# Kernel tuning notes

Hardware: AMD Instinct MI355X
Metric: run time of the kernel (lower is better)

The kernel has to match this reference:

```python
import jax, jax.numpy as jnp
import numpy as np

HINGES = 8_000_000
SHIMS = 2
L = 1.0


def setup_inputs() -> dict:
    key = jax.random.key(0)
    k1, k2, k3 = jax.random.split(key, 3)
    # straight chain [[0,0],[1,0],...] + small perturbation (as in _initiate_pos)
    x = jnp.arange(HINGES + 2, dtype=jnp.float32)
    base = jnp.stack([x, jnp.zeros_like(x)], axis=1)
    pos_arr = base + 0.01 * jax.random.normal(k1, (HINGES + 2, 2), dtype=jnp.float32)
    thetas_ss = 0.3 * jax.random.uniform(k2, (HINGES,), dtype=jnp.float32)
    rest_lengths = jnp.full((HINGES + 1,), L, dtype=jnp.float32)
    # buckle in {-1, +1}
    buckle = (2 * jax.random.randint(k3, (HINGES, SHIMS), 0, 2) - 1).astype(jnp.int32)
    return {
        "pos_arr": pos_arr,
        "thetas_ss": thetas_ss,
        "rest_lengths": rest_lengths,
        "k_stiff": jnp.asarray(10.0, dtype=jnp.float32),
        "k_soft": jnp.asarray(0.1, dtype=jnp.float32),
        "k_stretch": jnp.asarray(100.0, dtype=jnp.float32),
        "buckle": buckle,
    }


def _energy(pos, thetas_ss, rest_lengths, k_stiff, k_soft, k_stretch, buckle):
    # hinge angles: signed angle between consecutive edge vectors (vmap'd _get_theta)
    v1 = pos[1:-1] - pos[:-2]   # (H, 2)
    v2 = pos[2:] - pos[1:-1]    # (H, 2)
    cross = v1[:, 0] * v2[:, 1] - v1[:, 1] * v2[:, 0]
    dot = jnp.sum(v1 * v2, axis=-1)
    thetas = jnp.arctan2(cross, dot)             # (H,)
    # edge lengths (vmap'd _get_edge_length), edges = hinges + 1
    ev = pos[1:] - pos[:-1]
    edge_len = jnp.sqrt(jnp.sum(ev * ev, axis=-1))  # (H+1,)

    T = thetas[:, None]          # (H, 1)
    TH = thetas_ss[:, None]      # (H, 1)
    B = buckle                   # (H, shims)
    stiff_mask = ((B == 1) & (T > -TH)) | ((B == -1) & (T < TH))
    k_rot = jnp.where(stiff_mask, k_stiff, k_soft)
    rot_e = 0.5 * jnp.sum(k_rot * (T - TH) ** 2)
    str_e = 0.5 * jnp.sum(k_stretch * (edge_len - rest_lengths) ** 2)
    return rot_e + str_e, rot_e, str_e


def reference(pos_arr, thetas_ss, rest_lengths, k_stiff, k_soft, k_stretch, buckle):
    n_coords = pos_arr.size
    # nodes 0 and 1 (DOFs 0..3) are constrained per calculate_state
    free = jnp.ones((n_coords,), dtype=bool).at[:4].set(False)

    def total_E(x_flat):
        p = x_flat.reshape(pos_arr.shape)
        return _energy(p, thetas_ss, rest_lengths, k_stiff, k_soft, k_stretch, buckle)[0]

    g = jax.grad(total_E)(pos_arr.reshape(-1))
    force = jnp.where(free, -g, 0.0)             # -dE/dx on free DOFs

    tot, rot, st = _energy(pos_arr, thetas_ss, rest_lengths, k_stiff, k_soft, k_stretch, buckle)
    energies = jnp.stack([tot, rot, st])
    return jnp.concatenate([energies, force])
```

## Files before the change

kernel.cpp:

```cpp
#include <hip/hip_runtime.h>
#include <math.h>

#define TILE 256
#define PPT  4

__device__ __forceinline__ float fast_rcp(float x) { return __builtin_amdgcn_rcpf(x); }
__device__ __forceinline__ float fast_rsq(float x) { return __builtin_amdgcn_rsqf(x); }

__device__ __forceinline__ float atan_poly(float t) {
    const float c3 = -0.3333333333f, c5 = 0.2f, c7 = -0.1428571429f, c9 = 0.1111111111f;
    float t2 = t * t;
    return t * fmaf(t2, fmaf(t2, fmaf(t2, fmaf(t2, c9, c7), c5), c3), 1.0f);
}

__global__ __launch_bounds__(TILE) void hinge_chain_kernel(
    const float2* __restrict__ pos,
    const float*  __restrict__ thetas_ss,
    const float*  __restrict__ rest_len,
    const float*  __restrict__ k_stiff_p,
    const float*  __restrict__ k_soft_p,
    const float*  __restrict__ k_stretch_p,
    const int2*   __restrict__ buckle,
    float*        __restrict__ out,
    float2*       __restrict__ partials,
    int N)
{
    const int H = N - 2;
    const int E = N - 1;
    const int gid = blockIdx.x * TILE + threadIdx.x;
    const int p0  = gid * PPT;

    const float k_stiff   = *k_stiff_p;
    const float k_soft    = *k_soft_p;
    const float k_stretch = *k_stretch_p;

    float2 P[8];
    float  tss[6];
    int2   bb[6];
    float  rl[5];

    const bool interior = (p0 >= 2) && (p0 + 5 < N);
    if (interior) {
        const float4* p4 = reinterpret_cast<const float4*>(pos + (p0 - 2));
        float4 a = p4[0], b = p4[1], c = p4[2], d = p4[3];
        P[0] = make_float2(a.x, a.y); P[1] = make_float2(a.z, a.w);
        P[2] = make_float2(b.x, b.y); P[3] = make_float2(b.z, b.w);
        P[4] = make_float2(c.x, c.y); P[5] = make_float2(c.z, c.w);
        P[6] = make_float2(d.x, d.y); P[7] = make_float2(d.z, d.w);
        float2 t01 = *reinterpret_cast<const float2*>(thetas_ss + (p0 - 2));
        float4 t25 = *reinterpret_cast<const float4*>(thetas_ss + p0);
        tss[0] = t01.x; tss[1] = t01.y;
        tss[2] = t25.x; tss[3] = t25.y; tss[4] = t25.z; tss[5] = t25.w;
        rl[0] = rest_len[p0 - 1];
        float4 r14 = *reinterpret_cast<const float4*>(rest_len + p0);
        rl[1] = r14.x; rl[2] = r14.y; rl[3] = r14.z; rl[4] = r14.w;
        const int4* b4 = reinterpret_cast<const int4*>(buckle + (p0 - 2));
        int4 u = b4[0], v = b4[1], w = b4[2];
        bb[0] = make_int2(u.x, u.y); bb[1] = make_int2(u.z, u.w);
        bb[2] = make_int2(v.x, v.y); bb[3] = make_int2(v.z, v.w);
        bb[4] = make_int2(w.x, w.y); bb[5] = make_int2(w.z, w.w);
    } else {
        #pragma unroll
        for (int j = 0; j < 8; ++j) {
            int p = p0 - 2 + j;
            P[j] = (p >= 0 && p < N) ? pos[p] : make_float2(0.f, 0.f);
        }
        #pragma unroll
        for (int j = 0; j < 6; ++j) {
            int h = p0 - 2 + j;
            bool v = (h >= 0 && h < H);
            tss[j] = v ? thetas_ss[h] : 0.f;
            bb[j]  = v ? buckle[h]    : make_int2(0, 0);
        }
        #pragma unroll
        for (int k = 0; k < 5; ++k) {
            int e = p0 - 1 + k;
            rl[k] = (e >= 0 && e < E) ? rest_len[e] : 1.f;
        }
    }

    float rot_e = 0.f, str_e = 0.f;

    float2 g1[6], g2[6];
    #pragma unroll
    for (int j = 0; j < 6; ++j) {
        int h = p0 - 2 + j;
        bool valid = (h >= 0 && h < H);
        if (valid) {
            float2 a = P[j], b = P[j + 1], c = P[j + 2];
            float v1x = b.x - a.x, v1y = b.y - a.y;
            float v2x = c.x - b.x, v2y = c.y - b.y;
            float cr = v1x * v2y - v1y * v2x;
            float dt = v1x * v2x + v1y * v2y;
            float th;
            if (dt > 0.f) th = atan_poly(cr * fast_rcp(dt));
            else          th = atan2f(cr, dt);
            float ts  = tss[j];
            int2  bk  = bb[j];
            float dth = th - ts;
            bool m0 = (bk.x == 1 && th > -ts) || (bk.x == -1 && th < ts);
            bool m1 = (bk.y == 1 && th > -ts) || (bk.y == -1 && th < ts);
            float K = (m0 ? k_stiff : k_soft) + (m1 ? k_stiff : k_soft);
            if (j >= 2) rot_e += 0.5f * K * dth * dth;
            float gg  = K * dth;
            float inv = gg * fast_rcp(cr * cr + dt * dt);
            g1[j].x = inv * ( dt * v2y - cr * v2x);
            g1[j].y = inv * (-dt * v2x - cr * v2y);
            g2[j].x = inv * (-dt * v1y - cr * v1x);
            g2[j].y = inv * ( dt * v1x - cr * v1y);
        } else {
            g1[j] = make_float2(0.f, 0.f);
            g2[j] = make_float2(0.f, 0.f);
        }
    }

    float2 s[5];
    #pragma unroll
    for (int k = 0; k < 5; ++k) {
        int e = p0 - 1 + k;
        bool valid = (e >= 0 && e < E);
        if (valid) {
            float2 a = P[k + 1], b = P[k + 2];
            float ex = b.x - a.x, ey = b.y - a.y;
            float d2 = ex * ex + ey * ey;
            float invl = fast_rsq(d2);
            float len  = d2 * invl;
            float d    = len - rl[k];
            if (k >= 1) str_e += 0.5f * k_stretch * d * d;
            float cc = k_stretch * d * invl;
            s[k] = make_float2(cc * ex, cc * ey);
        } else {
            s[k] = make_float2(0.f, 0.f);
        }
    }

    #pragma unroll
    for (int m = 0; m < 4; ++m) {
        int p = p0 + m;
        if (p < N) {
            float gx = -g1[m + 2].x + g1[m + 1].x - g2[m + 1].x + g2[m].x + s[m].x - s[m + 1].x;
            float gy = -g1[m + 2].y + g1[m + 1].y - g2[m + 1].y + g2[m].y + s[m].y - s[m + 1].y;
            float fx = -gx, fy = -gy;
            if (p < 2) { fx = 0.f; fy = 0.f; }
            out[3 + 2 * p]     = fx;
            out[4 + 2 * p]     = fy;
        }
    }

    for (int off = 32; off > 0; off >>= 1) {
        rot_e += __shfl_down(rot_e, off);
        str_e += __shfl_down(str_e, off);
    }
    __shared__ float wr[TILE / 64], wsum[TILE / 64];
    int wave = threadIdx.x >> 6, lane = threadIdx.x & 63;
    if (lane == 0) { wr[wave] = rot_e; wsum[wave] = str_e; }
    __syncthreads();
    if (threadIdx.x == 0) {
        float r = 0.f, ss = 0.f;
        for (int w = 0; w < TILE / 64; ++w) { r += wr[w]; ss += wsum[w]; }
        partials[blockIdx.x] = make_float2(r, ss);
    }
}

__global__ __launch_bounds__(256) void reduce_partials_kernel(
    const float2* __restrict__ partials, int nblocks,
    float* __restrict__ out)
{
    const int tid = threadIdx.x;
    float r0 = 0.f, s0 = 0.f, r1 = 0.f, s1 = 0.f;
    int i = tid;
    for (; i + 256 < nblocks; i += 512) {
        float2 a = partials[i];
        float2 b = partials[i + 256];
        r0 += a.x; s0 += a.y;
        r1 += b.x; s1 += b.y;
    }
    if (i < nblocks) { float2 a = partials[i]; r0 += a.x; s0 += a.y; }
    float r = r0 + r1, s = s0 + s1;
    for (int off = 32; off > 0; off >>= 1) {
        r += __shfl_down(r, off);
        s += __shfl_down(s, off);
    }
    __shared__ float wr[4], wsv[4];
    int wave = tid >> 6, lane = tid & 63;
    if (lane == 0) { wr[wave] = r; wsv[wave] = s; }
    __syncthreads();
    if (tid == 0) {
        float R = 0.f, S = 0.f;
        for (int w = 0; w < 4; ++w) { R += wr[w]; S += wsv[w]; }
        out[0] = R + S;
        out[1] = R;
        out[2] = S;
    }
}

extern "C" void kernel_launch(void* const* d_in, const int* in_sizes, int n_in,
                              void* d_out, int out_size, void* d_ws, size_t ws_size,
                              hipStream_t stream) {
    const float2* pos       = (const float2*)d_in[0];
    const float*  thetas_ss = (const float*)d_in[1];
    const float*  rest_len  = (const float*)d_in[2];
    const float*  k_stiff   = (const float*)d_in[3];
    const float*  k_soft    = (const float*)d_in[4];
    const float*  k_stretch = (const float*)d_in[5];
    const int2*   buckle    = (const int2*)d_in[6];
    float*        out       = (float*)d_out;
    float2*       partials  = (float2*)d_ws;

    const int N = in_sizes[0] / 2;
    const int nthreads = (N + PPT - 1) / PPT;
    const int grid = (nthreads + TILE - 1) / TILE;

    hinge_chain_kernel<<<grid, TILE, 0, stream>>>(
        pos, thetas_ss, rest_len, k_stiff, k_soft, k_stretch, buckle, out, partials, N);

    reduce_partials_kernel<<<1, 256, 0, stream>>>(partials, grid, out);
}
```

Before: 223.8 us.

## Switch to persistent grid-stride loop with double-buffered chunk prefetch

Replaces the one-chunk-per-thread launch with a fixed grid of 1024 blocks that walk chunks in a grid-stride loop. Each thread loads the next chunk into a second register buffer while it computes the current one, so memory latency overlaps with math. The change also cuts the partials array and the final reduce work to 1024 entries. In exchange it roughly doubles register use per thread, which is capped through launch bounds and may cause spills or lower occupancy.

Measured after the change: 234.5 us. +4.8%, slower.

```diff
diff --git a/kernel.cpp b/kernel.cpp
--- a/kernel.cpp
+++ b/kernel.cpp
@@ -3,6 +3,7 @@
 
 #define TILE 256
 #define PPT  4
+#define NBLK 1024
 
 __device__ __forceinline__ float fast_rcp(float x) { return __builtin_amdgcn_rcpf(x); }
 __device__ __forceinline__ float fast_rsq(float x) { return __builtin_amdgcn_rsqf(x); }
@@ -13,73 +14,68 @@
     return t * fmaf(t2, fmaf(t2, fmaf(t2, fmaf(t2, c9, c7), c5), c3), 1.0f);
 }
 
-__global__ __launch_bounds__(TILE) void hinge_chain_kernel(
-    const float2* __restrict__ pos,
-    const float*  __restrict__ thetas_ss,
-    const float*  __restrict__ rest_len,
-    const float*  __restrict__ k_stiff_p,
-    const float*  __restrict__ k_soft_p,
-    const float*  __restrict__ k_stretch_p,
-    const int2*   __restrict__ buckle,
-    float*        __restrict__ out,
-    float2*       __restrict__ partials,
-    int N)
-{
-    const int H = N - 2;
-    const int E = N - 1;
-    const int gid = blockIdx.x * TILE + threadIdx.x;
-    const int p0  = gid * PPT;
-
-    const float k_stiff   = *k_stiff_p;
-    const float k_soft    = *k_soft_p;
-    const float k_stretch = *k_stretch_p;
-
+struct Chunk {
     float2 P[8];
     float  tss[6];
     int2   bb[6];
     float  rl[5];
-
+};
+
+__device__ __forceinline__ void loadChunk(
+    Chunk& ch, int c, int N, int H, int E,
+    const float2* __restrict__ pos,
+    const float*  __restrict__ thetas_ss,
+    const float*  __restrict__ rest_len,
+    const int2*   __restrict__ buckle)
+{
+    const int p0 = c * PPT;
     const bool interior = (p0 >= 2) && (p0 + 5 < N);
     if (interior) {
         const float4* p4 = reinterpret_cast<const float4*>(pos + (p0 - 2));
-        float4 a = p4[0], b = p4[1], c = p4[2], d = p4[3];
-        P[0] = make_float2(a.x, a.y); P[1] = make_float2(a.z, a.w);
-        P[2] = make_float2(b.x, b.y); P[3] = make_float2(b.z, b.w);
-        P[4] = make_float2(c.x, c.y); P[5] = make_float2(c.z, c.w);
-        P[6] = make_float2(d.x, d.y); P[7] = make_float2(d.z, d.w);
+        float4 a = p4[0], b = p4[1], cc = p4[2], d = p4[3];
+        ch.P[0] = make_float2(a.x, a.y);  ch.P[1] = make_float2(a.z, a.w);
+        ch.P[2] = make_float2(b.x, b.y);  ch.P[3] = make_float2(b.z, b.w);
+        ch.P[4] = make_float2(cc.x, cc.y); ch.P[5] = make_float2(cc.z, cc.w);
+        ch.P[6] = make_float2(d.x, d.y);  ch.P[7] = make_float2(d.z, d.w);
         float2 t01 = *reinterpret_cast<const float2*>(thetas_ss + (p0 - 2));
         float4 t25 = *reinterpret_cast<const float4*>(thetas_ss + p0);
-        tss[0] = t01.x; tss[1] = t01.y;
-        tss[2] = t25.x; tss[3] = t25.y; tss[4] = t25.z; tss[5] = t25.w;
-        rl[0] = rest_len[p0 - 1];
+        ch.tss[0] = t01.x; ch.tss[1] = t01.y;
+        ch.tss[2] = t25.x; ch.tss[3] = t25.y; ch.tss[4] = t25.z; ch.tss[5] = t25.w;
+        ch.rl[0] = rest_len[p0 - 1];
         float4 r14 = *reinterpret_cast<const float4*>(rest_len + p0);
-        rl[1] = r14.x; rl[2] = r14.y; rl[3] = r14.z; rl[4] = r14.w;
+        ch.rl[1] = r14.x; ch.rl[2] = r14.y; ch.rl[3] = r14.z; ch.rl[4] = r14.w;
         const int4* b4 = reinterpret_cast<const int4*>(buckle + (p0 - 2));
         int4 u = b4[0], v = b4[1], w = b4[2];
-        bb[0] = make_int2(u.x, u.y); bb[1] = make_int2(u.z, u.w);
-        bb[2] = make_int2(v.x, v.y); bb[3] = make_int2(v.z, v.w);
-        bb[4] = make_int2(w.x, w.y); bb[5] = make_int2(w.z, w.w);
+        ch.bb[0] = make_int2(u.x, u.y); ch.bb[1] = make_int2(u.z, u.w);
+        ch.bb[2] = make_int2(v.x, v.y); ch.bb[3] = make_int2(v.z, v.w);
+        ch.bb[4] = make_int2(w.x, w.y); ch.bb[5] = make_int2(w.z, w.w);
     } else {
         #pragma unroll
         for (int j = 0; j < 8; ++j) {
             int p = p0 - 2 + j;
-            P[j] = (p >= 0 && p < N) ? pos[p] : make_float2(0.f, 0.f);
+            ch.P[j] = (p >= 0 && p < N) ? pos[p] : make_float2(0.f, 0.f);
         }
         #pragma unroll
         for (int j = 0; j < 6; ++j) {
             int h = p0 - 2 + j;
             bool v = (h >= 0 && h < H);
-            tss[j] = v ? thetas_ss[h] : 0.f;
-            bb[j]  = v ? buckle[h]    : make_int2(0, 0);
+            ch.tss[j] = v ? thetas_ss[h] : 0.f;
+            ch.bb[j]  = v ? buckle[h]    : make_int2(0, 0);
         }
         #pragma unroll
         for (int k = 0; k < 5; ++k) {
             int e = p0 - 1 + k;
-            rl[k] = (e >= 0 && e < E) ? rest_len[e] : 1.f;
-        }
-    }
-
-    float rot_e = 0.f, str_e = 0.f;
+            ch.rl[k] = (e >= 0 && e < E) ? rest_len[e] : 1.f;
+        }
+    }
+}
+
+__device__ __forceinline__ void computeStore(
+    const Chunk& ch, int c, int N, int H, int E,
+    float k_stiff, float k_soft, float k_stretch,
+    float* __restrict__ out, float& rot_e, float& str_e)
+{
+    const int p0 = c * PPT;
 
     float2 g1[6], g2[6];
     #pragma unroll
@@ -87,16 +83,16 @@
         int h = p0 - 2 + j;
         bool valid = (h >= 0 && h < H);
         if (valid) {
-            float2 a = P[j], b = P[j + 1], c = P[j + 2];
-            float v1x = b.x - a.x, v1y = b.y - a.y;
-            float v2x = c.x - b.x, v2y = c.y - b.y;
+            float2 a = ch.P[j], b = ch.P[j + 1], cpt = ch.P[j + 2];
+            float v1x = b.x - a.x,   v1y = b.y - a.y;
+            float v2x = cpt.x - b.x, v2y = cpt.y - b.y;
             float cr = v1x * v2y - v1y * v2x;
             float dt = v1x * v2x + v1y * v2y;
             float th;
             if (dt > 0.f) th = atan_poly(cr * fast_rcp(dt));
             else          th = atan2f(cr, dt);
-            float ts  = tss[j];
-            int2  bk  = bb[j];
+            float ts  = ch.tss[j];
+            int2  bk  = ch.bb[j];
             float dth = th - ts;
             bool m0 = (bk.x == 1 && th > -ts) || (bk.x == -1 && th < ts);
             bool m1 = (bk.y == 1 && th > -ts) || (bk.y == -1 && th < ts);
@@ -120,12 +116,12 @@
         int e = p0 - 1 + k;
         bool valid = (e >= 0 && e < E);
         if (valid) {
-            float2 a = P[k + 1], b = P[k + 2];
+            float2 a = ch.P[k + 1], b = ch.P[k + 2];
             float ex = b.x - a.x, ey = b.y - a.y;
             float d2 = ex * ex + ey * ey;
             float invl = fast_rsq(d2);
             float len  = d2 * invl;
-            float d    = len - rl[k];
+            float d    = len - ch.rl[k];
             if (k >= 1) str_e += 0.5f * k_stretch * d * d;
             float cc = k_stretch * d * invl;
             s[k] = make_float2(cc * ex, cc * ey);
@@ -142,9 +138,53 @@
             float gy = -g1[m + 2].y + g1[m + 1].y - g2[m + 1].y + g2[m].y + s[m].y - s[m + 1].y;
             float fx = -gx, fy = -gy;
             if (p < 2) { fx = 0.f; fy = 0.f; }
-            out[3 + 2 * p]     = fx;
-            out[4 + 2 * p]     = fy;
-        }
+            out[3 + 2 * p] = fx;
+            out[4 + 2 * p] = fy;
+        }
+    }
+}
+
+__global__ __launch_bounds__(TILE, 4) void hinge_chain_kernel(
+    const float2* __restrict__ pos,
+    const float*  __restrict__ thetas_ss,
+    const float*  __restrict__ rest_len,
+    const float*  __restrict__ k_stiff_p,
+    const float*  __restrict__ k_soft_p,
+    const float*  __restrict__ k_stretch_p,
+    const int2*   __restrict__ buckle,
+    float*        __restrict__ out,
+    float2*       __restrict__ partials,
+    int N)
+{
+    const int H = N - 2;
+    const int E = N - 1;
+    const int C = (N + PPT - 1) / PPT;
+    const int T = gridDim.x * TILE;
+
+    const float k_stiff   = *k_stiff_p;
+    const float k_soft    = *k_soft_p;
+    const float k_stretch = *k_stretch_p;
+
+    float rot_e = 0.f, str_e = 0.f;
+
+    Chunk A, B;
+    int  c     = blockIdx.x * TILE + threadIdx.x;
+    bool valid = (c < C);
+    if (valid) loadChunk(A, c, N, H, E, pos, thetas_ss, rest_len, buckle);
+
+    while (valid) {
+        int  cn = c + T;
+        bool vn = (cn < C);
+        if (vn) loadChunk(B, cn, N, H, E, pos, thetas_ss, rest_len, buckle);
+        computeStore(A, c, N, H, E, k_stiff, k_soft, k_stretch, out, rot_e, str_e);
+        c = cn; valid = vn;
+        if (!valid) break;
+
+        cn = c + T;
+        vn = (cn < C);
+        if (vn) loadChunk(A, cn, N, H, E, pos, thetas_ss, rest_len, buckle);
+        computeStore(B, c, N, H, E, k_stiff, k_soft, k_stretch, out, rot_e, str_e);
+        c = cn; valid = vn;
     }
 
     for (int off = 32; off > 0; off >>= 1) {
@@ -208,8 +248,9 @@
     float2*       partials  = (float2*)d_ws;
 
     const int N = in_sizes[0] / 2;
-    const int nthreads = (N + PPT - 1) / PPT;
-    const int grid = (nthreads + TILE - 1) / TILE;
+    const int nchunks = (N + PPT - 1) / PPT;
+    int grid = NBLK;
+    if (grid * TILE > nchunks) grid = (nchunks + TILE - 1) / TILE;
 
     hinge_chain_kernel<<<grid, TILE, 0, stream>>>(
         pos, thetas_ss, rest_len, k_stiff, k_soft, k_stretch, buckle, out, partials, N);
```

## Stage block inputs into LDS via async global_load_lds before compute

Applied to the files above, without the earlier changes.

Each block now copies its whole span of positions, thetas, rest lengths and buckle values into shared memory using 16-byte global_load_lds transfers, with a guarded scalar fallback at the edges, then reads per-thread windows from LDS. This replaces overlapping per-thread global loads, where neighbouring threads re-fetch halo elements, with one coalesced bulk copy per block. In exchange it adds about 28 KB of LDS per block, which can lower occupancy, plus a barrier before compute. It also relies on the alignment and ordering semantics of the LDS-direct load.

After: 226.4 us. No clear change (+1.1%).

```diff
diff --git a/kernel.cpp b/kernel.cpp
--- a/kernel.cpp
+++ b/kernel.cpp
@@ -3,6 +3,12 @@
 
 #define TILE 256
 #define PPT  4
+#define SPAN (TILE * PPT)
+
+#define POS_CH 516
+#define TSS_CH 258
+#define RL_CH  258
+#define BB_CH  514
 
 __device__ __forceinline__ float fast_rcp(float x) { return __builtin_amdgcn_rcpf(x); }
 __device__ __forceinline__ float fast_rsq(float x) { return __builtin_amdgcn_rsqf(x); }
@@ -11,6 +17,12 @@
     const float c3 = -0.3333333333f, c5 = 0.2f, c7 = -0.1428571429f, c9 = 0.1111111111f;
     float t2 = t * t;
     return t * fmaf(t2, fmaf(t2, fmaf(t2, fmaf(t2, c9, c7), c5), c3), 1.0f);
+}
+
+__device__ __forceinline__ void gld16(const void* g, void* l) {
+    __builtin_amdgcn_global_load_lds(
+        (const __attribute__((address_space(1))) void*)g,
+        (__attribute__((address_space(3))) void*)l, 16, 0, 0);
 }
 
 __global__ __launch_bounds__(TILE) void hinge_chain_kernel(
@@ -27,56 +39,70 @@
 {
     const int H = N - 2;
     const int E = N - 1;
-    const int gid = blockIdx.x * TILE + threadIdx.x;
-    const int p0  = gid * PPT;
+    const int ltid = threadIdx.x;
+    const int Pb   = blockIdx.x * SPAN;
+    const int p0   = Pb + ltid * PPT;
 
     const float k_stiff   = *k_stiff_p;
     const float k_soft    = *k_soft_p;
     const float k_stretch = *k_stretch_p;
 
-    float2 P[8];
-    float  tss[6];
-    int2   bb[6];
-    float  rl[5];
-
-    const bool interior = (p0 >= 2) && (p0 + 5 < N);
-    if (interior) {
-        const float4* p4 = reinterpret_cast<const float4*>(pos + (p0 - 2));
-        float4 a = p4[0], b = p4[1], c = p4[2], d = p4[3];
+    __shared__ __align__(16) float2 lds_pos[1032];
+    __shared__ __align__(16) float  lds_tss[1032];
+    __shared__ __align__(16) float  lds_rl [1032];
+    __shared__ __align__(16) int2   lds_bb [1028];
+
+    const bool interiorBlk = (Pb >= 4) && (Pb + 1030 <= N);
+    if (interiorBlk) {
+        const char* gpos = (const char*)(pos       + (Pb - 2));
+        const char* gtss = (const char*)(thetas_ss + (Pb - 4));
+        const char* grl  = (const char*)(rest_len  + (Pb - 4));
+        const char* gbb  = (const char*)(buckle    + (Pb - 2));
+        char* lpos = (char*)lds_pos;
+        char* ltss = (char*)lds_tss;
+        char* lrl  = (char*)lds_rl;
+        char* lbb  = (char*)lds_bb;
+        for (int c = ltid; c < POS_CH; c += TILE) gld16(gpos + (size_t)c * 16, lpos + (c & ~63) * 16);
+        for (int c = ltid; c < BB_CH;  c += TILE) gld16(gbb  + (size_t)c * 16, lbb  + (c & ~63) * 16);
+        for (int c = ltid; c < TSS_CH; c += TILE) gld16(gtss + (size_t)c * 16, ltss + (c & ~63) * 16);
+        for (int c = ltid; c < RL_CH;  c += TILE) gld16(grl  + (size_t)c * 16, lrl  + (c & ~63) * 16);
+    } else {
+        for (int k = ltid; k < 1032; k += TILE) {
+            int p = Pb - 2 + k;
+            lds_pos[k] = (p >= 0 && p < N) ? pos[p] : make_float2(0.f, 0.f);
+            int h = Pb - 4 + k;
+            lds_tss[k] = (h >= 0 && h < H) ? thetas_ss[h] : 0.f;
+            int e = Pb - 4 + k;
+            lds_rl[k]  = (e >= 0 && e < E) ? rest_len[e] : 1.f;
+            if (k < 1028) {
+                int hb = Pb - 2 + k;
+                lds_bb[k] = (hb >= 0 && hb < H) ? buckle[hb] : make_int2(0, 0);
+            }
+        }
+    }
+    __syncthreads();
+
+    float2 P[8]; float tss[6]; int2 bb[6]; float rl[5];
+    {
+        const float4* pv = reinterpret_cast<const float4*>(lds_pos);
+        float4 a = pv[2 * ltid], b = pv[2 * ltid + 1], c = pv[2 * ltid + 2], d = pv[2 * ltid + 3];
         P[0] = make_float2(a.x, a.y); P[1] = make_float2(a.z, a.w);
         P[2] = make_float2(b.x, b.y); P[3] = make_float2(b.z, b.w);
         P[4] = make_float2(c.x, c.y); P[5] = make_float2(c.z, c.w);
         P[6] = make_float2(d.x, d.y); P[7] = make_float2(d.z, d.w);
-        float2 t01 = *reinterpret_cast<const float2*>(thetas_ss + (p0 - 2));
-        float4 t25 = *reinterpret_cast<const float4*>(thetas_ss + p0);
-        tss[0] = t01.x; tss[1] = t01.y;
-        tss[2] = t25.x; tss[3] = t25.y; tss[4] = t25.z; tss[5] = t25.w;
-        rl[0] = rest_len[p0 - 1];
-        float4 r14 = *reinterpret_cast<const float4*>(rest_len + p0);
-        rl[1] = r14.x; rl[2] = r14.y; rl[3] = r14.z; rl[4] = r14.w;
-        const int4* b4 = reinterpret_cast<const int4*>(buckle + (p0 - 2));
-        int4 u = b4[0], v = b4[1], w = b4[2];
+        float2 t0 = *reinterpret_cast<const float2*>(&lds_tss[4 * ltid + 2]);
+        float4 t1 = *reinterpret_cast<const float4*>(&lds_tss[4 * ltid + 4]);
+        tss[0] = t0.x; tss[1] = t0.y;
+        tss[2] = t1.x; tss[3] = t1.y; tss[4] = t1.z; tss[5] = t1.w;
+        float  r0 = lds_rl[4 * ltid + 3];
+        float4 r1 = *reinterpret_cast<const float4*>(&lds_rl[4 * ltid + 4]);
+        rl[0] = r0; rl[1] = r1.x; rl[2] = r1.y; rl[3] = r1.z; rl[4] = r1.w;
+        const int4* bv = reinterpret_cast<const int4*>(lds_bb);
+        int4 u = bv[2 * ltid], v = bv[2 * ltid + 1];
+        int2 w = *reinterpret_cast<const int2*>(&lds_bb[4 * ltid + 4]);
         bb[0] = make_int2(u.x, u.y); bb[1] = make_int2(u.z, u.w);
         bb[2] = make_int2(v.x, v.y); bb[3] = make_int2(v.z, v.w);
-        bb[4] = make_int2(w.x, w.y); bb[5] = make_int2(w.z, w.w);
-    } else {
-        #pragma unroll
-        for (int j = 0; j < 8; ++j) {
-            int p = p0 - 2 + j;
-            P[j] = (p >= 0 && p < N) ? pos[p] : make_float2(0.f, 0.f);
-        }
-        #pragma unroll
-        for (int j = 0; j < 6; ++j) {
-            int h = p0 - 2 + j;
-            bool v = (h >= 0 && h < H);
-            tss[j] = v ? thetas_ss[h] : 0.f;
-            bb[j]  = v ? buckle[h]    : make_int2(0, 0);
-        }
-        #pragma unroll
-        for (int k = 0; k < 5; ++k) {
-            int e = p0 - 1 + k;
-            rl[k] = (e >= 0 && e < E) ? rest_len[e] : 1.f;
-        }
+        bb[4] = w; bb[5] = *reinterpret_cast<const int2*>(&lds_bb[4 * ltid + 5]);
     }
 
     float rot_e = 0.f, str_e = 0.f;
@@ -142,8 +168,8 @@
             float gy = -g1[m + 2].y + g1[m + 1].y - g2[m + 1].y + g2[m].y + s[m].y - s[m + 1].y;
             float fx = -gx, fy = -gy;
             if (p < 2) { fx = 0.f; fy = 0.f; }
-            out[3 + 2 * p]     = fx;
-            out[4 + 2 * p]     = fy;
+            out[3 + 2 * p] = fx;
+            out[4 + 2 * p] = fy;
         }
     }
 
@@ -152,12 +178,12 @@
         str_e += __shfl_down(str_e, off);
     }
     __shared__ float wr[TILE / 64], wsum[TILE / 64];
-    int wave = threadIdx.x >> 6, lane = threadIdx.x & 63;
+    int wave = ltid >> 6, lane = ltid & 63;
     if (lane == 0) { wr[wave] = rot_e; wsum[wave] = str_e; }
     __syncthreads();
-    if (threadIdx.x == 0) {
+    if (ltid == 0) {
         float r = 0.f, ss = 0.f;
-        for (int w = 0; w < TILE / 64; ++w) { r += wr[w]; ss += wsum[w]; }
+        for (int w2 = 0; w2 < TILE / 64; ++w2) { r += wr[w2]; ss += wsum[w2]; }
         partials[blockIdx.x] = make_float2(r, ss);
     }
 }
```
